# Optimization experiments

Hardware: AMD Instinct MI355X
Metric: run time of the kernel (lower is better)

The kernel has to match this reference:

```python
import jax, jax.numpy as jnp
import numpy as np

B, T, DIM, NH = 2, 2048, 1024, 16
HD = DIM // NH  # 64


def setup_inputs() -> dict:
    key = jax.random.key(0)
    ks = jax.random.split(key, 5)
    x = jax.random.normal(ks[0], (B, T, DIM), dtype=jnp.float32)
    # realistic RoPE tables (any float tables work; use true rotary angles)
    inv_freq = 1.0 / (10000.0 ** (jnp.arange(0, HD, 2, dtype=jnp.float32) / HD))  # [HD/2]
    ang = jnp.arange(T, dtype=jnp.float32)[:, None] * inv_freq[None, :]           # [T, HD/2]
    ang = jnp.repeat(ang, 2, axis=-1)                                             # [T, HD] interleaved pairs
    sin = jnp.sin(ang)[None, None]  # [1,1,T,HD]
    cos = jnp.cos(ang)[None, None]
    W_qkv = jax.random.normal(ks[1], (DIM, 3 * DIM), dtype=jnp.float32) * (DIM ** -0.5)
    W_proj = jax.random.normal(ks[2], (DIM, DIM), dtype=jnp.float32) * (DIM ** -0.5)
    return {"x": x, "sin": sin, "cos": cos, "W_qkv": W_qkv, "W_proj": W_proj}


def _rope(x, sin, cos):
    # x: [B,H,T,D]; sin/cos: [1,1,T,D]
    x1, x2 = x[..., ::2], x[..., 1::2]
    xr = jnp.stack((-x2, x1), axis=-1).reshape(x.shape)  # interleave (-x2, x1)
    return x * cos + xr * sin


def reference(x, sin, cos, W_qkv, W_proj):
    Bx, Tx, C = x.shape
    nh, hd = NH, C // NH
    qkv = x @ W_qkv                                   # [B,T,3C]
    q, k, v = jnp.split(qkv, 3, axis=-1)
    to_bhtd = lambda t: t.reshape(Bx, Tx, nh, hd).transpose(0, 2, 1, 3)
    q, k, v = to_bhtd(q), to_bhtd(k), to_bhtd(v)      # [B,H,T,D]
    q = _rope(q, sin[:, :, :Tx], cos[:, :, :Tx])
    k = _rope(k, sin[:, :, :Tx], cos[:, :, :Tx])
    scale = 1.0 / jnp.sqrt(jnp.asarray(hd, dtype=x.dtype))
    scores = jnp.einsum('bhqd,bhkd->bhqk', q, k) * scale
    causal = jnp.tril(jnp.ones((Tx, Tx), dtype=bool))
    scores = jnp.where(causal, scores, jnp.finfo(scores.dtype).min)
    attn = jax.nn.softmax(scores, axis=-1)
    y = jnp.einsum('bhqk,bhkd->bhqd', attn, v)        # [B,H,T,D]
    y = y.transpose(0, 2, 1, 3).reshape(Bx, Tx, C)
    return y @ W_proj
```

## Files before the change

kernel.cpp:

```cpp
#include <hip/hip_runtime.h>


typedef float  f32x4  __attribute__((ext_vector_type(4)));
typedef __bf16 bf16x8 __attribute__((ext_vector_type(8)));
typedef short  short8 __attribute__((ext_vector_type(8)));

#define Bb   2
#define Tt   2048
#define DIMc 1024
#define NHh  16
#define HDd  64

__device__ __forceinline__ short f2bf(float f) {
    unsigned u = __builtin_bit_cast(unsigned, f);
    u += 0x7fffu + ((u >> 16) & 1u);
    return (short)(u >> 16);
}
__device__ __forceinline__ short f2bf_t(float f) {
    return (short)(__builtin_bit_cast(unsigned, f) >> 16);
}

__device__ __forceinline__ f32x4 mfma16(short8 a, short8 b, f32x4 c) {
    return __builtin_amdgcn_mfma_f32_16x16x32_bf16(
        __builtin_bit_cast(bf16x8, a), __builtin_bit_cast(bf16x8, b), c, 0, 0, 0);
}

__device__ __forceinline__ void gl_lds16(const void* g, void* l) {
    __builtin_amdgcn_global_load_lds(
        (const __attribute__((address_space(1))) unsigned int*)g,
        (__attribute__((address_space(3))) unsigned int*)l, 16, 0, 0);
}

__global__ __launch_bounds__(256) void prep(
    const float* __restrict__ X,  short* __restrict__ Xb,
    const float* __restrict__ Wq, short* __restrict__ Wqt,
    const float* __restrict__ Wp, short* __restrict__ Wpt)
{
    __shared__ float L[64][65];
    const int id = blockIdx.x, tid = threadIdx.x;
    if (id < 2048) {
        size_t i = ((size_t)id * 256 + tid) * 8;
        float4 a = *(const float4*)(X + i);
        float4 b = *(const float4*)(X + i + 4);
        short8 s;
        s[0] = f2bf(a.x); s[1] = f2bf(a.y); s[2] = f2bf(a.z); s[3] = f2bf(a.w);
        s[4] = f2bf(b.x); s[5] = f2bf(b.y); s[6] = f2bf(b.z); s[7] = f2bf(b.w);
        *(short8*)(Xb + i) = s;
        return;
    }
    const float* W; short* Wt; int N, id2;
    if (id < 2816) { W = Wq; Wt = Wqt; N = 3072; id2 = id - 2048; }
    else           { W = Wp; Wt = Wpt; N = 1024; id2 = id - 2816; }
    const int kb = (id2 & 15) * 64, nb = (id2 >> 4) * 64;
#pragma unroll
    for (int it = 0; it < 4; it++) {
        int kk = it * 16 + (tid >> 4), c = (tid & 15) * 4;
        float4 v = *(const float4*)(W + (size_t)(kb + kk) * N + nb + c);
        L[c + 0][kk] = v.x; L[c + 1][kk] = v.y;
        L[c + 2][kk] = v.z; L[c + 3][kk] = v.w;
    }
    __syncthreads();
#pragma unroll
    for (int it = 0; it < 2; it++) {
        int n = it * 32 + (tid >> 3), ks = (tid & 7) * 8;
        short8 s;
#pragma unroll
        for (int j = 0; j < 8; j++) s[j] = f2bf(L[n][ks + j]);
        *(short8*)(Wt + (size_t)(nb + n) * 1024 + kb + ks) = s;
    }
}

#define GEMM_BK32_LOOP(Aptr, Bptr)                                                \
    for (int k0 = 0; k0 < 1024; k0 += 32) {                                       \
        _Pragma("unroll")                                                         \
        for (int i = 0; i < 2; i++) {                                             \
            int p = tid + i * 256;                                                \
            int row = p >> 2, c = p & 3, gcs = (c ^ (row & 3)) * 8;               \
            gl_lds16(Aptr + (size_t)(bm * 128 + row) * 1024 + k0 + gcs,           \
                     &As[row][c * 8]);                                            \
        }                                                                         \
        _Pragma("unroll")                                                         \
        for (int i = 0; i < 2; i++) {                                             \
            int p = tid + i * 256;                                                \
            int row = p >> 2, c = p & 3, gcs = (c ^ (row & 3)) * 8;               \
            gl_lds16(Bptr + (size_t)(bn * 128 + row) * 1024 + k0 + gcs,           \
                     &Bs[row][c * 8]);                                            \
        }                                                                         \
        __syncthreads();                                                          \
        short8 af[4], bfr[4];                                                     \
        _Pragma("unroll")                                                         \
        for (int mt = 0; mt < 4; mt++)                                            \
            af[mt] = *(const short8*)&As[wr * 64 + mt * 16 + l16]                 \
                                       [(g ^ (l16 & 3)) * 8];                     \
        _Pragma("unroll")                                                         \
        for (int nt = 0; nt < 4; nt++)                                            \
            bfr[nt] = *(const short8*)&Bs[wc * 64 + nt * 16 + l16]                \
                                        [(g ^ (l16 & 3)) * 8];                    \
        _Pragma("unroll")                                                         \
        for (int mt = 0; mt < 4; mt++)                                            \
            _Pragma("unroll")                                                     \
            for (int nt = 0; nt < 4; nt++)                                        \
                acc[mt][nt] = mfma16(af[mt], bfr[nt], acc[mt][nt]);               \
        __syncthreads();                                                          \
    }

__global__ __launch_bounds__(256) void qkv_rope(
    const short* __restrict__ A, const short* __restrict__ Bt,
    const float* __restrict__ Sn, const float* __restrict__ Cs,
    short* __restrict__ Qo, short* __restrict__ Ko, short* __restrict__ Vt)
{
    __shared__ __align__(16) short As[128][32];
    __shared__ __align__(16) short Bs[128][32];
    const int bm = blockIdx.x, bn = blockIdx.y;
    const int tid = threadIdx.x;
    const int wv = tid >> 6, lane = tid & 63, g = lane >> 4, l16 = lane & 15;
    const int wr = wv >> 1, wc = wv & 1;

    f32x4 acc[4][4];
#pragma unroll
    for (int i = 0; i < 4; i++)
#pragma unroll
        for (int j = 0; j < 4; j++) acc[i][j] = (f32x4){0.f, 0.f, 0.f, 0.f};

    GEMM_BK32_LOOP(A, Bt)

#pragma unroll
    for (int mt = 0; mt < 4; mt++)
#pragma unroll
        for (int nt = 0; nt < 4; nt++)
#pragma unroll
            for (int r = 0; r < 4; r++) {
                int m = bm * 128 + wr * 64 + mt * 16 + g * 4 + r;
                int n = bn * 128 + wc * 64 + nt * 16 + l16;
                float val = acc[mt][nt][r];
                float partner = __shfl_xor(val, 1, 64);
                int b = m >> 11, t = m & 2047;
                int sec = n >> 10, nn = n & 1023;
                int h = nn >> 6, d = nn & 63;
                if (sec == 2) {
                    Vt[(((size_t)(b * 16 + h) * 64 + d) << 11) + t] = f2bf(val);
                } else {
                    float sv = Sn[t * 64 + d], cv = Cs[t * 64 + d];
                    float ro = (d & 1) ? fmaf(val, cv, partner * sv)
                                       : fmaf(val, cv, -partner * sv);
                    short* dst = (sec == 0) ? Qo : Ko;
                    dst[(((size_t)(b * 16 + h) << 11) + t) * 64 + d] = f2bf(ro);
                }
            }
}

__global__ __launch_bounds__(256, 4) void attn(
    const short* __restrict__ Q, const short* __restrict__ K,
    const short* __restrict__ V, short* __restrict__ Y)
{
    __shared__ __align__(16) short Ks[2][64][64];
    __shared__ __align__(16) short Vs[2][64][64];
    __shared__ __align__(16) short Pl[4][16][64];

    const int bh = blockIdx.y;
    const int tid = threadIdx.x, wv = tid >> 6, lane = tid & 63;
    const int g = lane >> 4, l16 = lane & 15;
    const short* Qb = Q + (size_t)bh * Tt * 64;
    const short* Kb = K + (size_t)bh * Tt * 64;
    const short* Vb = V + (size_t)bh * 64 * Tt;
    const int b = bh >> 4, h = bh & 15;

    const int rj = lane >> 3, cc = lane & 7, gc = cc ^ rj;
    const int sw = l16 & 7;

    short8 ones;
#pragma unroll
    for (int j = 0; j < 8; j++) ones[j] = (short)0x3F80;

    auto stage = [&](int s, int buf) {
        int k0s = s * 64;
#pragma unroll
        for (int j = 0; j < 2; j++) {
            int row = wv * 16 + j * 8 + rj;
            gl_lds16(Kb + (size_t)(k0s + row) * 64 + gc * 8, &Ks[buf][row][cc << 3]);
        }
#pragma unroll
        for (int j = 0; j < 2; j++) {
            int row = wv * 16 + j * 8 + rj;
            gl_lds16(Vb + (size_t)row * Tt + k0s + gc * 8, &Vs[buf][row][cc << 3]);
        }
    };

    for (int pass = 0; pass < 2; pass++) {
        const int qi = pass ? (31 - blockIdx.x) : blockIdx.x;
        const int q0w = qi * 64 + wv * 16;
        const int nsteps = qi + 1;

        short8 qf[2];
#pragma unroll
        for (int ss = 0; ss < 2; ss++)
            qf[ss] = *(const short8*)(Qb + (size_t)(q0w + l16) * 64 + ss * 32 + g * 8);

        f32x4 o[4], lacc = (f32x4){0.f, 0.f, 0.f, 0.f};
#pragma unroll
        for (int nt = 0; nt < 4; nt++) o[nt] = (f32x4){0.f, 0.f, 0.f, 0.f};

        __syncthreads();
        stage(0, 0);
        __syncthreads();

        for (int s = 0; s < nsteps; ++s) {
            if (s + 1 < nsteps) stage(s + 1, (s + 1) & 1);
            const int kb = s & 1, k0 = s * 64;

            f32x4 S[4];
#pragma unroll
            for (int t = 0; t < 4; t++) {
                S[t] = (f32x4){0.f, 0.f, 0.f, 0.f};
#pragma unroll
                for (int ss = 0; ss < 2; ss++) {
                    short8 kf = *(const short8*)&Ks[kb][t * 16 + l16][((ss * 4 + g) ^ sw) << 3];
                    S[t] = mfma16(qf[ss], kf, S[t]);
                }
            }

            float p[4][4];
            if (s < nsteps - 1) {
#pragma unroll
                for (int t = 0; t < 4; t++)
#pragma unroll
                    for (int r = 0; r < 4; r++)
                        p[t][r] = exp2f(fmaf(S[t][r], 0.18033688f, -14.4269504f));
            } else {
#pragma unroll
                for (int t = 0; t < 4; t++)
#pragma unroll
                    for (int r = 0; r < 4; r++) {
                        int key = k0 + t * 16 + l16, qq = q0w + g * 4 + r;
                        p[t][r] = (key <= qq)
                                  ? exp2f(fmaf(S[t][r], 0.18033688f, -14.4269504f)) : 0.f;
                    }
            }

#pragma unroll
            for (int t = 0; t < 4; t++)
#pragma unroll
                for (int r = 0; r < 4; r++) {
                    int row = g * 4 + r, c = t * 16 + l16;
                    Pl[wv][row][(((c >> 3) ^ (row & 7)) << 3) | (c & 7)] = f2bf_t(p[t][r]);
                }
            asm volatile("" ::: "memory");
            short8 pf[2];
#pragma unroll
            for (int ks = 0; ks < 2; ks++)
                pf[ks] = *(const short8*)&Pl[wv][l16][((ks * 4 + g) ^ sw) << 3];
#pragma unroll
            for (int ks = 0; ks < 2; ks++) {
                lacc = mfma16(pf[ks], ones, lacc);
#pragma unroll
                for (int nt = 0; nt < 4; nt++) {
                    short8 vf = *(const short8*)&Vs[kb][nt * 16 + l16][((ks * 4 + g) ^ sw) << 3];
                    o[nt] = mfma16(pf[ks], vf, o[nt]);
                }
            }
            __syncthreads();
        }

        float inv[4];
#pragma unroll
        for (int r = 0; r < 4; r++) inv[r] = 1.0f / lacc[r];
#pragma unroll
        for (int nt = 0; nt < 4; nt++)
#pragma unroll
            for (int r = 0; r < 4; r++) {
                int qq = q0w + g * 4 + r, d = nt * 16 + l16;
                Y[((size_t)(b * Tt + qq)) * DIMc + h * 64 + d] = f2bf(o[nt][r] * inv[r]);
            }
    }
}

__global__ __launch_bounds__(256) void proj(
    const short* __restrict__ A, const short* __restrict__ Bt, float* __restrict__ O)
{
    __shared__ __align__(16) short As[128][32];
    __shared__ __align__(16) short Bs[128][32];
    const int bm = blockIdx.x, bn = blockIdx.y;
    const int tid = threadIdx.x;
    const int wv = tid >> 6, lane = tid & 63, g = lane >> 4, l16 = lane & 15;
    const int wr = wv >> 1, wc = wv & 1;

    f32x4 acc[4][4];
#pragma unroll
    for (int i = 0; i < 4; i++)
#pragma unroll
        for (int j = 0; j < 4; j++) acc[i][j] = (f32x4){0.f, 0.f, 0.f, 0.f};

    GEMM_BK32_LOOP(A, Bt)

#pragma unroll
    for (int mt = 0; mt < 4; mt++)
#pragma unroll
        for (int nt = 0; nt < 4; nt++)
#pragma unroll
            for (int r = 0; r < 4; r++) {
                int m = bm * 128 + wr * 64 + mt * 16 + g * 4 + r;
                int n = bn * 128 + wc * 64 + nt * 16 + l16;
                O[(size_t)m * 1024 + n] = acc[mt][nt][r];
            }
}

extern "C" void kernel_launch(void* const* d_in, const int* in_sizes, int n_in,
                              void* d_out, int out_size, void* d_ws, size_t ws_size,
                              hipStream_t stream)
{
    const float* x     = (const float*)d_in[0];
    const float* sn    = (const float*)d_in[1];
    const float* cs    = (const float*)d_in[2];
    const float* wqkv  = (const float*)d_in[3];
    const float* wproj = (const float*)d_in[4];
    float* out = (float*)d_out;

    char* ws = (char*)d_ws;
    const size_t MB = 1024 * 1024;
    short* q   = (short*)(ws);
    short* k   = (short*)(ws + 8  * MB);
    short* vt  = (short*)(ws + 16 * MB);
    short* y   = (short*)(ws + 24 * MB);
    short* xb  = (short*)(ws + 32 * MB);
    short* wqt = (short*)(ws + 40 * MB);
    short* wpt = (short*)(ws + 46 * MB);

    prep<<<3072, 256, 0, stream>>>(x, xb, wqkv, wqt, wproj, wpt);
    qkv_rope<<<dim3(32, 24), 256, 0, stream>>>(xb, wqt, sn, cs, q, k, vt);
    attn<<<dim3(16, Bb * NHh), 256, 0, stream>>>(q, k, vt, y);
    proj<<<dim3(32, 8), 256, 0, stream>>>(y, wpt, out);
}
```

Baseline: 208.8 us.

## Use 128-row query tiles per block with register-staged K/V prefetch

The attention kernel now gives each block one 128-query tile, with each wave handling 32 rows as two 16-row subtiles. The old scheme ran two 64-row passes per block over paired tiles. K/V fragments read from LDS are now reused across both query subtiles, which halves LDS reads of K and V per query row. The async global-to-LDS copies are replaced by register preloads that are committed to LDS after compute, and the launch bound drops to 2 blocks per CU. Causal load balance now comes from the blockIdx.y bit rather than from pairing passes, and the higher register use and coarser tiles may reduce occupancy and balance.

```diff
diff --git a/kernel.cpp b/kernel.cpp
--- a/kernel.cpp
+++ b/kernel.cpp
@@ -149,15 +149,16 @@
             }
 }
 
-__global__ __launch_bounds__(256, 4) void attn(
+__global__ __launch_bounds__(256, 2) void attn(
     const short* __restrict__ Q, const short* __restrict__ K,
     const short* __restrict__ V, short* __restrict__ Y)
 {
     __shared__ __align__(16) short Ks[2][64][64];
     __shared__ __align__(16) short Vs[2][64][64];
-    __shared__ __align__(16) short Pl[4][16][64];
+    __shared__ __align__(16) short Pl[4][32][64];
 
     const int bh = blockIdx.y;
+    const int qi = (blockIdx.y & 16) ? (15 - blockIdx.x) : blockIdx.x;
     const int tid = threadIdx.x, wv = tid >> 6, lane = tid & 63;
     const int g = lane >> 4, l16 = lane & 15;
     const short* Qb = Q + (size_t)bh * Tt * 64;
@@ -167,109 +168,141 @@
 
     const int rj = lane >> 3, cc = lane & 7, gc = cc ^ rj;
     const int sw = l16 & 7;
+    const int q0w = qi * 128 + wv * 32;
 
     short8 ones;
 #pragma unroll
     for (int j = 0; j < 8; j++) ones[j] = (short)0x3F80;
 
-    auto stage = [&](int s, int buf) {
-        int k0s = s * 64;
+    short8 kp[2], vp[2];
+    auto preload = [&](int s) {
 #pragma unroll
         for (int j = 0; j < 2; j++) {
             int row = wv * 16 + j * 8 + rj;
-            gl_lds16(Kb + (size_t)(k0s + row) * 64 + gc * 8, &Ks[buf][row][cc << 3]);
+            kp[j] = *(const short8*)(Kb + (size_t)(s * 64 + row) * 64 + gc * 8);
+            vp[j] = *(const short8*)(Vb + (size_t)row * Tt + s * 64 + gc * 8);
         }
+    };
+    auto commit = [&](int buf) {
 #pragma unroll
         for (int j = 0; j < 2; j++) {
             int row = wv * 16 + j * 8 + rj;
-            gl_lds16(Vb + (size_t)row * Tt + k0s + gc * 8, &Vs[buf][row][cc << 3]);
+            *(short8*)&Ks[buf][row][cc << 3] = kp[j];
+            *(short8*)&Vs[buf][row][cc << 3] = vp[j];
         }
     };
 
-    for (int pass = 0; pass < 2; pass++) {
-        const int qi = pass ? (31 - blockIdx.x) : blockIdx.x;
-        const int q0w = qi * 64 + wv * 16;
-        const int nsteps = qi + 1;
-
-        short8 qf[2];
+    short8 qf[2][2];
+#pragma unroll
+    for (int qs = 0; qs < 2; qs++)
 #pragma unroll
         for (int ss = 0; ss < 2; ss++)
-            qf[ss] = *(const short8*)(Qb + (size_t)(q0w + l16) * 64 + ss * 32 + g * 8);
-
-        f32x4 o[4], lacc = (f32x4){0.f, 0.f, 0.f, 0.f};
-#pragma unroll
-        for (int nt = 0; nt < 4; nt++) o[nt] = (f32x4){0.f, 0.f, 0.f, 0.f};
-
+            qf[qs][ss] = *(const short8*)(Qb + (size_t)(q0w + qs * 16 + l16) * 64
+                                             + ss * 32 + g * 8);
+
+    f32x4 o[2][4], lacc[2];
+#pragma unroll
+    for (int qs = 0; qs < 2; qs++) {
+        lacc[qs] = (f32x4){0.f, 0.f, 0.f, 0.f};
+#pragma unroll
+        for (int nt = 0; nt < 4; nt++) o[qs][nt] = (f32x4){0.f, 0.f, 0.f, 0.f};
+    }
+
+    const int nsteps = 2 * (qi + 1);
+    preload(0); commit(0);
+    __syncthreads();
+
+    for (int s = 0; s < nsteps; ++s) {
+        const int kb = s & 1, k0 = s * 64;
+        const bool more = (s + 1 < nsteps);
+        if (more) preload(s + 1);
+
+        if (k0 <= q0w + 31) {
+            const bool diag = (k0 + 64 > q0w);
+            short8 kf[2][4];
+#pragma unroll
+            for (int ss = 0; ss < 2; ss++)
+#pragma unroll
+                for (int t = 0; t < 4; t++)
+                    kf[ss][t] = *(const short8*)&Ks[kb][t * 16 + l16]
+                                                   [((ss * 4 + g) ^ sw) << 3];
+#pragma unroll
+            for (int qs = 0; qs < 2; qs++) {
+                f32x4 S[4];
+#pragma unroll
+                for (int t = 0; t < 4; t++) {
+                    S[t] = (f32x4){0.f, 0.f, 0.f, 0.f};
+#pragma unroll
+                    for (int ss = 0; ss < 2; ss++)
+                        S[t] = mfma16(qf[qs][ss], kf[ss][t], S[t]);
+                }
+                float p[4][4];
+                if (!diag) {
+#pragma unroll
+                    for (int t = 0; t < 4; t++)
+#pragma unroll
+                        for (int r = 0; r < 4; r++)
+                            p[t][r] = exp2f(fmaf(S[t][r], 0.18033688f, -14.4269504f));
+                } else {
+#pragma unroll
+                    for (int t = 0; t < 4; t++)
+#pragma unroll
+                        for (int r = 0; r < 4; r++) {
+                            int key = k0 + t * 16 + l16;
+                            int qq  = q0w + qs * 16 + g * 4 + r;
+                            p[t][r] = (key <= qq)
+                                ? exp2f(fmaf(S[t][r], 0.18033688f, -14.4269504f)) : 0.f;
+                        }
+                }
+#pragma unroll
+                for (int t = 0; t < 4; t++)
+#pragma unroll
+                    for (int r = 0; r < 4; r++) {
+                        int row = qs * 16 + g * 4 + r, c = t * 16 + l16;
+                        Pl[wv][row][(((c >> 3) ^ (row & 7)) << 3) | (c & 7)] =
+                            f2bf_t(p[t][r]);
+                    }
+            }
+            asm volatile("" ::: "memory");
+            short8 vf[2][4];
+#pragma unroll
+            for (int ks = 0; ks < 2; ks++)
+#pragma unroll
+                for (int nt = 0; nt < 4; nt++)
+                    vf[ks][nt] = *(const short8*)&Vs[kb][nt * 16 + l16]
+                                                    [((ks * 4 + g) ^ sw) << 3];
+#pragma unroll
+            for (int qs = 0; qs < 2; qs++) {
+                short8 pf[2];
+#pragma unroll
+                for (int ks = 0; ks < 2; ks++)
+                    pf[ks] = *(const short8*)&Pl[wv][qs * 16 + l16]
+                                                [((ks * 4 + g) ^ sw) << 3];
+#pragma unroll
+                for (int ks = 0; ks < 2; ks++) {
+                    lacc[qs] = mfma16(pf[ks], ones, lacc[qs]);
+#pragma unroll
+                    for (int nt = 0; nt < 4; nt++)
+                        o[qs][nt] = mfma16(pf[ks], vf[ks][nt], o[qs][nt]);
+                }
+            }
+        }
+        if (more) commit((s + 1) & 1);
         __syncthreads();
-        stage(0, 0);
-        __syncthreads();
-
-        for (int s = 0; s < nsteps; ++s) {
-            if (s + 1 < nsteps) stage(s + 1, (s + 1) & 1);
-            const int kb = s & 1, k0 = s * 64;
-
-            f32x4 S[4];
-#pragma unroll
-            for (int t = 0; t < 4; t++) {
-                S[t] = (f32x4){0.f, 0.f, 0.f, 0.f};
-#pragma unroll
-                for (int ss = 0; ss < 2; ss++) {
-                    short8 kf = *(const short8*)&Ks[kb][t * 16 + l16][((ss * 4 + g) ^ sw) << 3];
-                    S[t] = mfma16(qf[ss], kf, S[t]);
-                }
-            }
-
-            float p[4][4];
-            if (s < nsteps - 1) {
-#pragma unroll
-                for (int t = 0; t < 4; t++)
-#pragma unroll
-                    for (int r = 0; r < 4; r++)
-                        p[t][r] = exp2f(fmaf(S[t][r], 0.18033688f, -14.4269504f));
-            } else {
-#pragma unroll
-                for (int t = 0; t < 4; t++)
-#pragma unroll
-                    for (int r = 0; r < 4; r++) {
-                        int key = k0 + t * 16 + l16, qq = q0w + g * 4 + r;
-                        p[t][r] = (key <= qq)
-                                  ? exp2f(fmaf(S[t][r], 0.18033688f, -14.4269504f)) : 0.f;
-                    }
-            }
-
-#pragma unroll
-            for (int t = 0; t < 4; t++)
-#pragma unroll
-                for (int r = 0; r < 4; r++) {
-                    int row = g * 4 + r, c = t * 16 + l16;
-                    Pl[wv][row][(((c >> 3) ^ (row & 7)) << 3) | (c & 7)] = f2bf_t(p[t][r]);
-                }
-            asm volatile("" ::: "memory");
-            short8 pf[2];
-#pragma unroll
-            for (int ks = 0; ks < 2; ks++)
-                pf[ks] = *(const short8*)&Pl[wv][l16][((ks * 4 + g) ^ sw) << 3];
-#pragma unroll
-            for (int ks = 0; ks < 2; ks++) {
-                lacc = mfma16(pf[ks], ones, lacc);
-#pragma unroll
-                for (int nt = 0; nt < 4; nt++) {
-                    short8 vf = *(const short8*)&Vs[kb][nt * 16 + l16][((ks * 4 + g) ^ sw) << 3];
-                    o[nt] = mfma16(pf[ks], vf, o[nt]);
-                }
-            }
-            __syncthreads();
-        }
-
+    }
+
+#pragma unroll
+    for (int qs = 0; qs < 2; qs++) {
         float inv[4];
 #pragma unroll
-        for (int r = 0; r < 4; r++) inv[r] = 1.0f / lacc[r];
+        for (int r = 0; r < 4; r++) inv[r] = 1.0f / lacc[qs][r];
 #pragma unroll
         for (int nt = 0; nt < 4; nt++)
 #pragma unroll
             for (int r = 0; r < 4; r++) {
-                int qq = q0w + g * 4 + r, d = nt * 16 + l16;
-                Y[((size_t)(b * Tt + qq)) * DIMc + h * 64 + d] = f2bf(o[nt][r] * inv[r]);
+                int qq = q0w + qs * 16 + g * 4 + r, d = nt * 16 + l16;
+                Y[((size_t)(b * Tt + qq)) * DIMc + h * 64 + d] =
+                    f2bf(o[qs][nt][r] * inv[r]);
             }
     }
 }
```

After: 207.9 us. About the same (-0.4%).

## Fuse all stages into one persistent kernel with grid barriers and work queue

Applied to the files above, without the earlier changes.

Replaces the four launches (prep, qkv+rope, attention, projection) with a single persistent kernel of 768 blocks separated by atomic grid-wide barriers. Attention tiles are pulled from an atomic work counter in longest-first order instead of fixed two-pass pairing, and K/V staging switches from async global-to-LDS double buffering to register prefetch into a single LDS buffer. The aim is to remove launch gaps and tail imbalance between stages. In exchange it relies on all 768 blocks being co-resident (a deadlock risk if occupancy falls short), adds barrier spin cost, and leaves most blocks idle during the projection phase.

```diff
diff --git a/kernel.cpp b/kernel.cpp
--- a/kernel.cpp
+++ b/kernel.cpp
@@ -1,15 +1,13 @@
 #include <hip/hip_runtime.h>
 
 
-typedef float  f32x4  __attribute__((ext_vector_type(4)));
-typedef __bf16 bf16x8 __attribute__((ext_vector_type(8)));
-typedef short  short8 __attribute__((ext_vector_type(8)));
-
-#define Bb   2
-#define Tt   2048
-#define DIMc 1024
-#define NHh  16
-#define HDd  64
+typedef float  f32x4   __attribute__((ext_vector_type(4)));
+typedef __bf16 bf16x8  __attribute__((ext_vector_type(8)));
+typedef short  short8  __attribute__((ext_vector_type(8)));
+typedef short  short4v __attribute__((ext_vector_type(4)));
+
+#define Tt 2048
+#define NBLK 768u
 
 __device__ __forceinline__ short f2bf(float f) {
     unsigned u = __builtin_bit_cast(unsigned, f);
@@ -19,55 +17,29 @@
 __device__ __forceinline__ short f2bf_t(float f) {
     return (short)(__builtin_bit_cast(unsigned, f) >> 16);
 }
-
 __device__ __forceinline__ f32x4 mfma16(short8 a, short8 b, f32x4 c) {
     return __builtin_amdgcn_mfma_f32_16x16x32_bf16(
         __builtin_bit_cast(bf16x8, a), __builtin_bit_cast(bf16x8, b), c, 0, 0, 0);
 }
-
 __device__ __forceinline__ void gl_lds16(const void* g, void* l) {
     __builtin_amdgcn_global_load_lds(
         (const __attribute__((address_space(1))) unsigned int*)g,
         (__attribute__((address_space(3))) unsigned int*)l, 16, 0, 0);
 }
 
-__global__ __launch_bounds__(256) void prep(
-    const float* __restrict__ X,  short* __restrict__ Xb,
-    const float* __restrict__ Wq, short* __restrict__ Wqt,
-    const float* __restrict__ Wp, short* __restrict__ Wpt)
-{
-    __shared__ float L[64][65];
-    const int id = blockIdx.x, tid = threadIdx.x;
-    if (id < 2048) {
-        size_t i = ((size_t)id * 256 + tid) * 8;
-        float4 a = *(const float4*)(X + i);
-        float4 b = *(const float4*)(X + i + 4);
-        short8 s;
-        s[0] = f2bf(a.x); s[1] = f2bf(a.y); s[2] = f2bf(a.z); s[3] = f2bf(a.w);
-        s[4] = f2bf(b.x); s[5] = f2bf(b.y); s[6] = f2bf(b.z); s[7] = f2bf(b.w);
-        *(short8*)(Xb + i) = s;
-        return;
-    }
-    const float* W; short* Wt; int N, id2;
-    if (id < 2816) { W = Wq; Wt = Wqt; N = 3072; id2 = id - 2048; }
-    else           { W = Wp; Wt = Wpt; N = 1024; id2 = id - 2816; }
-    const int kb = (id2 & 15) * 64, nb = (id2 >> 4) * 64;
-#pragma unroll
-    for (int it = 0; it < 4; it++) {
-        int kk = it * 16 + (tid >> 4), c = (tid & 15) * 4;
-        float4 v = *(const float4*)(W + (size_t)(kb + kk) * N + nb + c);
-        L[c + 0][kk] = v.x; L[c + 1][kk] = v.y;
-        L[c + 2][kk] = v.z; L[c + 3][kk] = v.w;
-    }
+__device__ __forceinline__ void gbar(unsigned* B) {
     __syncthreads();
-#pragma unroll
-    for (int it = 0; it < 2; it++) {
-        int n = it * 32 + (tid >> 3), ks = (tid & 7) * 8;
-        short8 s;
-#pragma unroll
-        for (int j = 0; j < 8; j++) s[j] = f2bf(L[n][ks + j]);
-        *(short8*)(Wt + (size_t)(nb + n) * 1024 + kb + ks) = s;
-    }
+    if (threadIdx.x == 0) {
+        __threadfence();
+        __hip_atomic_fetch_add(B, 1u, __ATOMIC_RELEASE, __HIP_MEMORY_SCOPE_AGENT);
+        while (__hip_atomic_load(B, __ATOMIC_ACQUIRE, __HIP_MEMORY_SCOPE_AGENT) < NBLK)
+            __builtin_amdgcn_s_sleep(2);
+    }
+    __syncthreads();
+}
+
+__global__ void zinit(unsigned* p) {
+    if (threadIdx.x < 8) p[threadIdx.x] = 0u;
 }
 
 #define GEMM_BK32_LOOP(Aptr, Bptr)                                                \
@@ -104,204 +76,232 @@
         __syncthreads();                                                          \
     }
 
-__global__ __launch_bounds__(256) void qkv_rope(
-    const short* __restrict__ A, const short* __restrict__ Bt,
-    const float* __restrict__ Sn, const float* __restrict__ Cs,
-    short* __restrict__ Qo, short* __restrict__ Ko, short* __restrict__ Vt)
+__global__ __launch_bounds__(256, 4) void fused(
+    const float* __restrict__ X,  const float* __restrict__ Sn,
+    const float* __restrict__ Cs, const float* __restrict__ Wq,
+    const float* __restrict__ Wp, float* __restrict__ Out,
+    short* __restrict__ Qg, short* __restrict__ Kg, short* __restrict__ Vg,
+    short* __restrict__ Yg, short* __restrict__ Xb,
+    short* __restrict__ Wqt, short* __restrict__ Wpt,
+    unsigned* __restrict__ sync)
 {
-    __shared__ __align__(16) short As[128][32];
-    __shared__ __align__(16) short Bs[128][32];
-    const int bm = blockIdx.x, bn = blockIdx.y;
-    const int tid = threadIdx.x;
+    __shared__ __align__(16) char smem[25600];
+    __shared__ unsigned su;
+    const int blk = blockIdx.x, tid = threadIdx.x;
     const int wv = tid >> 6, lane = tid & 63, g = lane >> 4, l16 = lane & 15;
-    const int wr = wv >> 1, wc = wv & 1;
-
-    f32x4 acc[4][4];
-#pragma unroll
-    for (int i = 0; i < 4; i++)
-#pragma unroll
-        for (int j = 0; j < 4; j++) acc[i][j] = (f32x4){0.f, 0.f, 0.f, 0.f};
-
-    GEMM_BK32_LOOP(A, Bt)
-
-#pragma unroll
-    for (int mt = 0; mt < 4; mt++)
-#pragma unroll
-        for (int nt = 0; nt < 4; nt++)
-#pragma unroll
-            for (int r = 0; r < 4; r++) {
-                int m = bm * 128 + wr * 64 + mt * 16 + g * 4 + r;
-                int n = bn * 128 + wc * 64 + nt * 16 + l16;
-                float val = acc[mt][nt][r];
-                float partner = __shfl_xor(val, 1, 64);
-                int b = m >> 11, t = m & 2047;
-                int sec = n >> 10, nn = n & 1023;
-                int h = nn >> 6, d = nn & 63;
-                if (sec == 2) {
-                    Vt[(((size_t)(b * 16 + h) * 64 + d) << 11) + t] = f2bf(val);
-                } else {
-                    float sv = Sn[t * 64 + d], cv = Cs[t * 64 + d];
-                    float ro = (d & 1) ? fmaf(val, cv, partner * sv)
-                                       : fmaf(val, cv, -partner * sv);
-                    short* dst = (sec == 0) ? Qo : Ko;
-                    dst[(((size_t)(b * 16 + h) << 11) + t) * 64 + d] = f2bf(ro);
+
+    {
+        float (*L)[65] = (float(*)[65])smem;
+        for (int u = blk; u < 3072; u += 768) {
+            if (u < 2048) {
+                size_t i = ((size_t)u * 256 + tid) * 8;
+                float4 a = *(const float4*)(X + i);
+                float4 b = *(const float4*)(X + i + 4);
+                short8 s;
+                s[0] = f2bf(a.x); s[1] = f2bf(a.y); s[2] = f2bf(a.z); s[3] = f2bf(a.w);
+                s[4] = f2bf(b.x); s[5] = f2bf(b.y); s[6] = f2bf(b.z); s[7] = f2bf(b.w);
+                *(short8*)(Xb + i) = s;
+            } else {
+                const float* W; short* Wt; int N, id2;
+                if (u < 2816) { W = Wq; Wt = Wqt; N = 3072; id2 = u - 2048; }
+                else          { W = Wp; Wt = Wpt; N = 1024; id2 = u - 2816; }
+                const int kb = (id2 & 15) * 64, nb = (id2 >> 4) * 64;
+                __syncthreads();
+#pragma unroll
+                for (int it = 0; it < 4; it++) {
+                    int kk = it * 16 + (tid >> 4), c = (tid & 15) * 4;
+                    float4 v = *(const float4*)(W + (size_t)(kb + kk) * N + nb + c);
+                    L[c + 0][kk] = v.x; L[c + 1][kk] = v.y;
+                    L[c + 2][kk] = v.z; L[c + 3][kk] = v.w;
+                }
+                __syncthreads();
+#pragma unroll
+                for (int it = 0; it < 2; it++) {
+                    int n = it * 32 + (tid >> 3), ks = (tid & 7) * 8;
+                    short8 s;
+#pragma unroll
+                    for (int j = 0; j < 8; j++) s[j] = f2bf(L[n][ks + j]);
+                    *(short8*)(Wt + (size_t)(nb + n) * 1024 + kb + ks) = s;
                 }
             }
-}
-
-__global__ __launch_bounds__(256, 4) void attn(
-    const short* __restrict__ Q, const short* __restrict__ K,
-    const short* __restrict__ V, short* __restrict__ Y)
-{
-    __shared__ __align__(16) short Ks[2][64][64];
-    __shared__ __align__(16) short Vs[2][64][64];
-    __shared__ __align__(16) short Pl[4][16][64];
-
-    const int bh = blockIdx.y;
-    const int tid = threadIdx.x, wv = tid >> 6, lane = tid & 63;
-    const int g = lane >> 4, l16 = lane & 15;
-    const short* Qb = Q + (size_t)bh * Tt * 64;
-    const short* Kb = K + (size_t)bh * Tt * 64;
-    const short* Vb = V + (size_t)bh * 64 * Tt;
-    const int b = bh >> 4, h = bh & 15;
-
-    const int rj = lane >> 3, cc = lane & 7, gc = cc ^ rj;
-    const int sw = l16 & 7;
-
-    short8 ones;
-#pragma unroll
-    for (int j = 0; j < 8; j++) ones[j] = (short)0x3F80;
-
-    auto stage = [&](int s, int buf) {
-        int k0s = s * 64;
-#pragma unroll
-        for (int j = 0; j < 2; j++) {
-            int row = wv * 16 + j * 8 + rj;
-            gl_lds16(Kb + (size_t)(k0s + row) * 64 + gc * 8, &Ks[buf][row][cc << 3]);
         }
-#pragma unroll
-        for (int j = 0; j < 2; j++) {
-            int row = wv * 16 + j * 8 + rj;
-            gl_lds16(Vb + (size_t)row * Tt + k0s + gc * 8, &Vs[buf][row][cc << 3]);
+    }
+    gbar(&sync[0]);
+
+    {
+        short (*As)[32] = (short(*)[32])smem;
+        short (*Bs)[32] = (short(*)[32])(smem + 8192);
+        const int bm = blk & 31, bn = blk >> 5;
+        const int wr = wv >> 1, wc = wv & 1;
+        f32x4 acc[4][4];
+#pragma unroll
+        for (int i = 0; i < 4; i++)
+#pragma unroll
+            for (int j = 0; j < 4; j++) acc[i][j] = (f32x4){0.f, 0.f, 0.f, 0.f};
+
+        GEMM_BK32_LOOP(Xb, Wqt)
+
+#pragma unroll
+        for (int mt = 0; mt < 4; mt++)
+#pragma unroll
+            for (int nt = 0; nt < 4; nt++)
+#pragma unroll
+                for (int r = 0; r < 4; r++) {
+                    int m = bm * 128 + wr * 64 + mt * 16 + g * 4 + r;
+                    int n = bn * 128 + wc * 64 + nt * 16 + l16;
+                    float val = acc[mt][nt][r];
+                    float partner = __shfl_xor(val, 1, 64);
+                    int b = m >> 11, t = m & 2047;
+                    int sec = n >> 10, nn = n & 1023;
+                    int h = nn >> 6, d = nn & 63;
+                    if (sec == 2) {
+                        Vg[(((size_t)(b * 16 + h) * 64 + d) << 11) + t] = f2bf(val);
+                    } else {
+                        float sv = Sn[t * 64 + d], cv = Cs[t * 64 + d];
+                        float ro = (d & 1) ? fmaf(val, cv, partner * sv)
+                                           : fmaf(val, cv, -partner * sv);
+                        short* dst = (sec == 0) ? Qg : Kg;
+                        dst[(((size_t)(b * 16 + h) << 11) + t) * 64 + d] = f2bf(ro);
+                    }
+                }
+    }
+    gbar(&sync[1]);
+
+    {
+        short (*Ks)[64] = (short(*)[64])smem;
+        short (*Vs)[64] = (short(*)[64])(smem + 8192);
+        short* Plw = (short*)(smem + 16384) + wv * 16 * 72;
+        const int rj = lane >> 3, cc = lane & 7, gc = cc ^ rj;
+        const int sw = l16 & 7;
+        short8 ones;
+#pragma unroll
+        for (int j = 0; j < 8; j++) ones[j] = (short)0x3F80;
+
+        for (;;) {
+            __syncthreads();
+            if (tid == 0)
+                su = __hip_atomic_fetch_add(&sync[3], 1u, __ATOMIC_RELAXED,
+                                            __HIP_MEMORY_SCOPE_AGENT);
+            __syncthreads();
+            unsigned u = su;
+            if (u >= 1024u) break;
+            const int bh = (int)(u & 31u);
+            const int qi = 31 - (int)(u >> 5);
+            const short* Qb = Qg + (size_t)bh * Tt * 64;
+            const short* Kb = Kg + (size_t)bh * Tt * 64;
+            const short* Vb = Vg + (size_t)bh * 64 * Tt;
+            const int b = bh >> 4, h = bh & 15;
+            const int q0w = qi * 64 + wv * 16;
+
+            short8 qf[2];
+#pragma unroll
+            for (int ss = 0; ss < 2; ss++)
+                qf[ss] = *(const short8*)(Qb + (size_t)(q0w + l16) * 64 + ss * 32 + g * 8);
+
+            f32x4 o[4], lacc = (f32x4){0.f, 0.f, 0.f, 0.f};
+#pragma unroll
+            for (int nt = 0; nt < 4; nt++) o[nt] = (f32x4){0.f, 0.f, 0.f, 0.f};
+
+            const int nsteps = qi + 1;
+            short8 kp[2], vp[2];
+            auto preload = [&](int s) {
+#pragma unroll
+                for (int j = 0; j < 2; j++) {
+                    int row = wv * 16 + j * 8 + rj;
+                    kp[j] = *(const short8*)(Kb + (size_t)(s * 64 + row) * 64 + gc * 8);
+                    vp[j] = *(const short8*)(Vb + (size_t)row * Tt + s * 64 + gc * 8);
+                }
+            };
+            auto commit = [&]() {
+#pragma unroll
+                for (int j = 0; j < 2; j++) {
+                    int row = wv * 16 + j * 8 + rj;
+                    *(short8*)&Ks[row][cc << 3] = kp[j];
+                    *(short8*)&Vs[row][cc << 3] = vp[j];
+                }
+            };
+
+            preload(0); commit();
+            __syncthreads();
+
+            for (int s = 0; s < nsteps; ++s) {
+                if (s + 1 < nsteps) preload(s + 1);
+                const int k0 = s * 64;
+                const bool diag = (s == qi);
+#pragma unroll
+                for (int t = 0; t < 4; t++) {
+                    f32x4 S = (f32x4){0.f, 0.f, 0.f, 0.f};
+#pragma unroll
+                    for (int ss = 0; ss < 2; ss++) {
+                        short8 kf = *(const short8*)&Ks[t * 16 + l16][((ss * 4 + g) ^ sw) << 3];
+                        S = mfma16(kf, qf[ss], S);
+                    }
+                    short4v pk;
+#pragma unroll
+                    for (int r = 0; r < 4; r++) {
+                        float e = exp2f(fmaf(S[r], 0.18033688f, -14.4269504f));
+                        if (diag && (k0 + t * 16 + g * 4 + r > q0w + l16)) e = 0.f;
+                        pk[r] = f2bf_t(e);
+                    }
+                    *(short4v*)&Plw[l16 * 72 + t * 16 + g * 4] = pk;
+                }
+                asm volatile("" ::: "memory");
+                short8 pf[2];
+#pragma unroll
+                for (int ks = 0; ks < 2; ks++)
+                    pf[ks] = *(const short8*)&Plw[l16 * 72 + ks * 32 + g * 8];
+#pragma unroll
+                for (int ks = 0; ks < 2; ks++) {
+                    lacc = mfma16(pf[ks], ones, lacc);
+#pragma unroll
+                    for (int nt = 0; nt < 4; nt++) {
+                        short8 vf = *(const short8*)&Vs[nt * 16 + l16][((ks * 4 + g) ^ sw) << 3];
+                        o[nt] = mfma16(pf[ks], vf, o[nt]);
+                    }
+                }
+                __syncthreads();
+                if (s + 1 < nsteps) { commit(); __syncthreads(); }
+            }
+
+            float inv[4];
+#pragma unroll
+            for (int r = 0; r < 4; r++) inv[r] = 1.0f / lacc[r];
+#pragma unroll
+            for (int nt = 0; nt < 4; nt++)
+#pragma unroll
+                for (int r = 0; r < 4; r++) {
+                    int qq = q0w + g * 4 + r, d = nt * 16 + l16;
+                    Yg[((size_t)(b * Tt + qq)) * 1024 + h * 64 + d] =
+                        f2bf(o[nt][r] * inv[r]);
+                }
         }
-    };
-
-    for (int pass = 0; pass < 2; pass++) {
-        const int qi = pass ? (31 - blockIdx.x) : blockIdx.x;
-        const int q0w = qi * 64 + wv * 16;
-        const int nsteps = qi + 1;
-
-        short8 qf[2];
-#pragma unroll
-        for (int ss = 0; ss < 2; ss++)
-            qf[ss] = *(const short8*)(Qb + (size_t)(q0w + l16) * 64 + ss * 32 + g * 8);
-
-        f32x4 o[4], lacc = (f32x4){0.f, 0.f, 0.f, 0.f};
-#pragma unroll
-        for (int nt = 0; nt < 4; nt++) o[nt] = (f32x4){0.f, 0.f, 0.f, 0.f};
-
-        __syncthreads();
-        stage(0, 0);
-        __syncthreads();
-
-        for (int s = 0; s < nsteps; ++s) {
-            if (s + 1 < nsteps) stage(s + 1, (s + 1) & 1);
-            const int kb = s & 1, k0 = s * 64;
-
-            f32x4 S[4];
-#pragma unroll
-            for (int t = 0; t < 4; t++) {
-                S[t] = (f32x4){0.f, 0.f, 0.f, 0.f};
-#pragma unroll
-                for (int ss = 0; ss < 2; ss++) {
-                    short8 kf = *(const short8*)&Ks[kb][t * 16 + l16][((ss * 4 + g) ^ sw) << 3];
-                    S[t] = mfma16(qf[ss], kf, S[t]);
-                }
-            }
-
-            float p[4][4];
-            if (s < nsteps - 1) {
-#pragma unroll
-                for (int t = 0; t < 4; t++)
-#pragma unroll
-                    for (int r = 0; r < 4; r++)
-                        p[t][r] = exp2f(fmaf(S[t][r], 0.18033688f, -14.4269504f));
-            } else {
-#pragma unroll
-                for (int t = 0; t < 4; t++)
-#pragma unroll
-                    for (int r = 0; r < 4; r++) {
-                        int key = k0 + t * 16 + l16, qq = q0w + g * 4 + r;
-                        p[t][r] = (key <= qq)
-                                  ? exp2f(fmaf(S[t][r], 0.18033688f, -14.4269504f)) : 0.f;
-                    }
-            }
-
-#pragma unroll
-            for (int t = 0; t < 4; t++)
+    }
+    gbar(&sync[2]);
+
+    if (blk < 256) {
+        short (*As)[32] = (short(*)[32])smem;
+        short (*Bs)[32] = (short(*)[32])(smem + 8192);
+        const int bm = blk & 31, bn = blk >> 5;
+        const int wr = wv >> 1, wc = wv & 1;
+        f32x4 acc[4][4];
+#pragma unroll
+        for (int i = 0; i < 4; i++)
+#pragma unroll
+            for (int j = 0; j < 4; j++) acc[i][j] = (f32x4){0.f, 0.f, 0.f, 0.f};
+
+        GEMM_BK32_LOOP(Yg, Wpt)
+
+#pragma unroll
+        for (int mt = 0; mt < 4; mt++)
+#pragma unroll
+            for (int nt = 0; nt < 4; nt++)
 #pragma unroll
                 for (int r = 0; r < 4; r++) {
-                    int row = g * 4 + r, c = t * 16 + l16;
-                    Pl[wv][row][(((c >> 3) ^ (row & 7)) << 3) | (c & 7)] = f2bf_t(p[t][r]);
-                }
-            asm volatile("" ::: "memory");
-            short8 pf[2];
-#pragma unroll
-            for (int ks = 0; ks < 2; ks++)
-                pf[ks] = *(const short8*)&Pl[wv][l16][((ks * 4 + g) ^ sw) << 3];
-#pragma unroll
-            for (int ks = 0; ks < 2; ks++) {
-                lacc = mfma16(pf[ks], ones, lacc);
-#pragma unroll
-                for (int nt = 0; nt < 4; nt++) {
-                    short8 vf = *(const short8*)&Vs[kb][nt * 16 + l16][((ks * 4 + g) ^ sw) << 3];
-                    o[nt] = mfma16(pf[ks], vf, o[nt]);
-                }
-            }
-            __syncthreads();
-        }
-
-        float inv[4];
-#pragma unroll
-        for (int r = 0; r < 4; r++) inv[r] = 1.0f / lacc[r];
-#pragma unroll
-        for (int nt = 0; nt < 4; nt++)
-#pragma unroll
-            for (int r = 0; r < 4; r++) {
-                int qq = q0w + g * 4 + r, d = nt * 16 + l16;
-                Y[((size_t)(b * Tt + qq)) * DIMc + h * 64 + d] = f2bf(o[nt][r] * inv[r]);
-            }
-    }
-}
-
-__global__ __launch_bounds__(256) void proj(
-    const short* __restrict__ A, const short* __restrict__ Bt, float* __restrict__ O)
-{
-    __shared__ __align__(16) short As[128][32];
-    __shared__ __align__(16) short Bs[128][32];
-    const int bm = blockIdx.x, bn = blockIdx.y;
-    const int tid = threadIdx.x;
-    const int wv = tid >> 6, lane = tid & 63, g = lane >> 4, l16 = lane & 15;
-    const int wr = wv >> 1, wc = wv & 1;
-
-    f32x4 acc[4][4];
-#pragma unroll
-    for (int i = 0; i < 4; i++)
-#pragma unroll
-        for (int j = 0; j < 4; j++) acc[i][j] = (f32x4){0.f, 0.f, 0.f, 0.f};
-
-    GEMM_BK32_LOOP(A, Bt)
-
-#pragma unroll
-    for (int mt = 0; mt < 4; mt++)
-#pragma unroll
-        for (int nt = 0; nt < 4; nt++)
-#pragma unroll
-            for (int r = 0; r < 4; r++) {
-                int m = bm * 128 + wr * 64 + mt * 16 + g * 4 + r;
-                int n = bn * 128 + wc * 64 + nt * 16 + l16;
-                O[(size_t)m * 1024 + n] = acc[mt][nt][r];
-            }
+                    int m = bm * 128 + wr * 64 + mt * 16 + g * 4 + r;
+                    int n = bn * 128 + wc * 64 + nt * 16 + l16;
+                    Out[(size_t)m * 1024 + n] = acc[mt][nt][r];
+                }
+    }
 }
 
 extern "C" void kernel_launch(void* const* d_in, const int* in_sizes, int n_in,
@@ -317,16 +317,16 @@
 
     char* ws = (char*)d_ws;
     const size_t MB = 1024 * 1024;
-    short* q   = (short*)(ws);
-    short* k   = (short*)(ws + 8  * MB);
-    short* vt  = (short*)(ws + 16 * MB);
-    short* y   = (short*)(ws + 24 * MB);
-    short* xb  = (short*)(ws + 32 * MB);
-    short* wqt = (short*)(ws + 40 * MB);
-    short* wpt = (short*)(ws + 46 * MB);
-
-    prep<<<3072, 256, 0, stream>>>(x, xb, wqkv, wqt, wproj, wpt);
-    qkv_rope<<<dim3(32, 24), 256, 0, stream>>>(xb, wqt, sn, cs, q, k, vt);
-    attn<<<dim3(16, Bb * NHh), 256, 0, stream>>>(q, k, vt, y);
-    proj<<<dim3(32, 8), 256, 0, stream>>>(y, wpt, out);
-}
+    short* q    = (short*)(ws);
+    short* k    = (short*)(ws + 8  * MB);
+    short* vt   = (short*)(ws + 16 * MB);
+    short* y    = (short*)(ws + 24 * MB);
+    short* xb   = (short*)(ws + 32 * MB);
+    short* wqt  = (short*)(ws + 40 * MB);
+    short* wpt  = (short*)(ws + 46 * MB);
+    unsigned* sy = (unsigned*)(ws + 48 * MB);
+
+    zinit<<<1, 64, 0, stream>>>(sy);
+    fused<<<768, 256, 0, stream>>>(x, sn, cs, wqkv, wproj, out,
+                                   q, k, vt, y, xb, wqt, wpt, sy);
+}
```

Measured after the change: 680.5 us. 226% more time.
